# Optimization experiments

Measured on AMD Instinct MI355X. Metric: run time of the kernel, lower is better.

The kernel has to match this reference:

```python
import jax, jax.numpy as jnp
import numpy as np

N = 50000      # nodes
E = 800000     # edges (avg degree 16)
IN = 128       # in_channels
OUT = 128      # out_channels


def setup_inputs() -> dict:
    key = jax.random.key(0)
    k1, k2, k3 = jax.random.split(key, 3)
    x = jax.random.normal(k1, (N, IN), dtype=jnp.float32)
    edge_index = jax.random.randint(k2, (2, E), 0, N, dtype=jnp.int32)
    # GCNConv params: glorot-ish linear weight + zero bias
    W = jax.random.normal(k3, (IN, OUT), dtype=jnp.float32) / np.float32(np.sqrt(IN))
    b = jnp.zeros((OUT,), dtype=jnp.float32)
    return {"x": x, "W": W, "b": b, "edge_index": edge_index}


def reference(x, W, b, edge_index):
    n = x.shape[0]
    src, dst = edge_index[0], edge_index[1]
    # add self loops (GCNConv default add_self_loops=True)
    loop = jnp.arange(n, dtype=edge_index.dtype)
    src = jnp.concatenate([src, loop])
    dst = jnp.concatenate([dst, loop])
    # symmetric normalization: deg^{-1/2}[src] * deg^{-1/2}[dst], deg from dst (flow source_to_target)
    deg = jax.ops.segment_sum(jnp.ones_like(dst, dtype=x.dtype), dst, num_segments=n)
    dinv = jnp.where(deg > 0, jax.lax.rsqrt(jnp.maximum(deg, 1.0)), 0.0)
    norm = dinv[src] * dinv[dst]                     # [E+N]
    xw = x @ W                                       # [N, OUT] dense GEMM first (as GCNConv does)
    msg = xw[src] * norm[:, None]                    # [E+N, OUT] gather + scale
    out = jax.ops.segment_sum(msg, dst, num_segments=n)  # scatter-add aggregate
    return out + b
```

## Files before the change

### kernel.cpp

```cpp
#include <hip/hip_runtime.h>


constexpr int CH = 128;
constexpr int CHUNK = 4096;
constexpr int NCMAX = 256;
constexpr int HP = 256;

typedef __attribute__((ext_vector_type(8))) short short8;
typedef __attribute__((ext_vector_type(4))) float f32x4;

static __device__ __forceinline__ ushort f2bf(float f) {
    unsigned u = __float_as_uint(f);
    u += 0x7fff + ((u >> 16) & 1);
    return (ushort)(u >> 16);
}


__global__ __launch_bounds__(256) void hist_kernel(const int* __restrict__ dst,
        int* __restrict__ h, int* __restrict__ coltot, int E, int nc, int nblk) {
    __shared__ int hh[NCMAX];
    int t = threadIdx.x, b = blockIdx.x;
    for (int i = t; i < NCMAX; i += 256) hh[i] = 0;
    __syncthreads();
    int s = b * CHUNK, e = min(E, s + CHUNK);
    for (int i = s + t * 4; i < e; i += 1024) {
        if (i + 4 <= e) {
            int4 v = *(const int4*)&dst[i];
            atomicAdd(&hh[v.x >> 8], 1);
            atomicAdd(&hh[v.y >> 8], 1);
            atomicAdd(&hh[v.z >> 8], 1);
            atomicAdd(&hh[v.w >> 8], 1);
        } else {
            for (int k = i; k < e; ++k) atomicAdd(&hh[dst[k] >> 8], 1);
        }
    }
    __syncthreads();
    for (int i = t; i < nc; i += 256) {
        int v = hh[i];
        h[(size_t)i * HP + b] = v;
        if (v) atomicAdd(&coltot[i], v);
    }
}

__global__ __launch_bounds__(256) void binscatter_kernel(const int* __restrict__ src,
        const int* __restrict__ dst, const int* __restrict__ h,
        const int* __restrict__ coltot, unsigned* __restrict__ ebuf,
        int E, int nc, int nblk) {
    __shared__ int smc[256];
    __shared__ int cur[NCMAX];
    int t = threadIdx.x, b = blockIdx.x;

    smc[t] = (t < nc) ? coltot[t] : 0;
    __syncthreads();
    #pragma unroll
    for (int d = 1; d < 256; d <<= 1) {
        int u = (t >= d) ? smc[t - d] : 0;
        __syncthreads();
        smc[t] += u;
        __syncthreads();
    }
    if (t < nc) {
        int base = (t > 0) ? smc[t - 1] : 0;
        const int* hp = &h[(size_t)t * HP];
        int pfx = 0;
        int j = 0;
        for (; j + 4 <= b; j += 4) {
            int4 v = *(const int4*)&hp[j];
            pfx += v.x + v.y + v.z + v.w;
        }
        for (; j < b; ++j) pfx += hp[j];
        cur[t] = base + pfx;
    }
    __syncthreads();
    int s = b * CHUNK, e = min(E, s + CHUNK);
    for (int i = s + t; i < e; i += 256) {
        int d = dst[i];
        int pos = atomicAdd(&cur[d >> 8], 1);
        ebuf[pos] = (unsigned)src[i] | ((unsigned)(d & 255) << 16);
    }
}

__global__ __launch_bounds__(256) void bucket_csr_packw(const unsigned* __restrict__ ebuf,
        const int* __restrict__ coltot, int* __restrict__ off, ushort* __restrict__ csr,
        float* __restrict__ dinv, const float* __restrict__ Wm, ushort* __restrict__ Wp,
        int N, int nc) {
    __shared__ int hist2[256], cur[256], sm[256];
    int t = threadIdx.x, k = blockIdx.x;
    if (k >= nc) {
        int tid = (k - nc) * 256 + t;
        if (tid < 2048) {
            int col = tid >> 4, ch16 = tid & 15;
            ushort tmp[8];
            #pragma unroll
            for (int i = 0; i < 8; ++i)
                tmp[i] = f2bf(Wm[(size_t)(ch16 * 8 + i) * CH + col]);
            int d = col * 16 + (ch16 ^ (col & 7));
            *(uint4*)&Wp[(size_t)d * 8] = *(uint4*)tmp;
        }
        return;
    }
    sm[t] = (t < nc) ? coltot[t] : 0;
    __syncthreads();
    #pragma unroll
    for (int d = 1; d < 256; d <<= 1) {
        int u = (t >= d) ? sm[t - d] : 0;
        __syncthreads();
        sm[t] += u;
        __syncthreads();
    }
    int s = (k > 0) ? sm[k - 1] : 0;
    int e = sm[k];
    __syncthreads();

    hist2[t] = 0;
    __syncthreads();
    for (int i = s + t; i < e; i += 256) atomicAdd(&hist2[(ebuf[i] >> 16) & 255], 1);
    __syncthreads();
    int v = hist2[t];
    sm[t] = v;
    __syncthreads();
    #pragma unroll
    for (int d = 1; d < 256; d <<= 1) {
        int u = (t >= d) ? sm[t - d] : 0;
        __syncthreads();
        sm[t] += u;
        __syncthreads();
    }
    int excl = sm[t] - v;
    int node = k * 256 + t;
    if (node <= N) off[node] = s + excl;
    if (node < N) dinv[node] = rsqrtf((float)(v + 1));
    cur[t] = s + excl;
    __syncthreads();
    for (int i = s + t; i < e; i += 256) {
        unsigned u = ebuf[i];
        int pos = atomicAdd(&cur[(u >> 16) & 255], 1);
        csr[pos] = (ushort)(u & 0xffffu);
    }
}


__global__ __launch_bounds__(256) void gemm_mfma(const float* __restrict__ x,
        const ushort* __restrict__ Wp, const float* __restrict__ dinv,
        ushort* __restrict__ xwd, int N) {
    __shared__ alignas(16) ushort Wlds[16384];
    int t = threadIdx.x;
    int wv = t >> 6, l = t & 63;
    int c15 = l & 15, kc = l >> 4;
    int row0 = blockIdx.x * 64 + wv * 16;
    int r = row0 + c15;
    bool valid = r < N;

    short8 af[4];
    #pragma unroll
    for (int ks = 0; ks < 4; ++ks) {
        float4 a0 = make_float4(0.f,0.f,0.f,0.f), a1 = a0;
        if (valid) {
            const float* p = x + (size_t)r * CH + ks * 32 + kc * 8;
            a0 = *(const float4*)p;
            a1 = *(const float4*)(p + 4);
        }
        short8 v;
        v[0]=f2bf(a0.x); v[1]=f2bf(a0.y); v[2]=f2bf(a0.z); v[3]=f2bf(a0.w);
        v[4]=f2bf(a1.x); v[5]=f2bf(a1.y); v[6]=f2bf(a1.z); v[7]=f2bf(a1.w);
        af[ks] = v;
    }

    #pragma unroll
    for (int i = 0; i < 8; ++i) {
        int idx = i * 256 + t;
        *(uint4*)&Wlds[idx * 8] = *(const uint4*)&Wp[idx * 8];
    }
    __syncthreads();

    f32x4 acc[8];
    #pragma unroll
    for (int ct = 0; ct < 8; ++ct) { f32x4 z = {0.f,0.f,0.f,0.f}; acc[ct] = z; }

    int swz = l & 7;
    #pragma unroll
    for (int ks = 0; ks < 4; ++ks) {
        #pragma unroll
        for (int ct = 0; ct < 8; ++ct) {
            int col = ct * 16 + c15;
            int idx16 = (col * 16 + ks * 4 + kc) ^ swz;
            short8 bfrag = *(const short8*)&Wlds[idx16 * 8];
            acc[ct] = __builtin_amdgcn_mfma_f32_16x16x32_bf16(af[ks], bfrag, acc[ct], 0, 0, 0);
        }
    }

    float dv[4];
    #pragma unroll
    for (int rr = 0; rr < 4; ++rr) {
        int row = row0 + kc * 4 + rr;
        dv[rr] = (row < N) ? dinv[row] : 0.f;
    }
    __syncthreads();

    ushort* bw = Wlds + wv * 2048;
    #pragma unroll
    for (int ct = 0; ct < 8; ++ct) {
        #pragma unroll
        for (int rr = 0; rr < 4; ++rr) {
            int row_local = kc * 4 + rr;
            bw[row_local * CH + ct * 16 + c15] = f2bf(acc[ct][rr] * dv[rr]);
        }
    }
    #pragma unroll
    for (int p = 0; p < 4; ++p) {
        int row_local = p * 4 + kc;
        int row = row0 + row_local;
        if (row < N) {
            uint4 vv = *(const uint4*)&bw[row_local * CH + c15 * 8];
            *(uint4*)&xwd[(size_t)row * CH + c15 * 8] = vv;
        }
    }
}


__global__ __launch_bounds__(256) void agg_kernel(const ushort* __restrict__ xwd,
        const ushort* __restrict__ csr, const int* __restrict__ off,
        const float* __restrict__ dinv, const float* __restrict__ b,
        float* __restrict__ out, int N) {
    int t = threadIdx.x;
    int c15 = t & 15;
    int node = blockIdx.x * 16 + (t >> 4);
    if (node >= N) return;
    int s = off[node], e = off[node + 1];
    float acc[8] = {0.f,0.f,0.f,0.f,0.f,0.f,0.f,0.f};
    const ushort* base = xwd + c15 * 8;

    int last = e - 1;
    for (int j = s; j < e; j += 8) {
        int idx[8]; float m[8];
        #pragma unroll
        for (int k = 0; k < 8; ++k) {
            int jj = j + k;
            idx[k] = csr[min(jj, last)];
            m[k] = (jj <= last) ? 1.0f : 0.0f;
        }
        uint4 v[8];
        #pragma unroll
        for (int k = 0; k < 8; ++k)
            v[k] = *(const uint4*)(base + (size_t)idx[k] * CH);
        #pragma unroll
        for (int k = 0; k < 8; ++k) {
            acc[0] += m[k] * __uint_as_float(v[k].x << 16);
            acc[1] += m[k] * __uint_as_float(v[k].x & 0xffff0000u);
            acc[2] += m[k] * __uint_as_float(v[k].y << 16);
            acc[3] += m[k] * __uint_as_float(v[k].y & 0xffff0000u);
            acc[4] += m[k] * __uint_as_float(v[k].z << 16);
            acc[5] += m[k] * __uint_as_float(v[k].z & 0xffff0000u);
            acc[6] += m[k] * __uint_as_float(v[k].w << 16);
            acc[7] += m[k] * __uint_as_float(v[k].w & 0xffff0000u);
        }
    }
    {
        uint4 v = *(const uint4*)(base + (size_t)node * CH);
        acc[0] += __uint_as_float(v.x << 16);
        acc[1] += __uint_as_float(v.x & 0xffff0000u);
        acc[2] += __uint_as_float(v.y << 16);
        acc[3] += __uint_as_float(v.y & 0xffff0000u);
        acc[4] += __uint_as_float(v.z << 16);
        acc[5] += __uint_as_float(v.z & 0xffff0000u);
        acc[6] += __uint_as_float(v.w << 16);
        acc[7] += __uint_as_float(v.w & 0xffff0000u);
    }
    float di = dinv[node];
    float4 b0 = *(const float4*)&b[c15 * 8];
    float4 b1 = *(const float4*)&b[c15 * 8 + 4];
    f32x4 o0, o1;
    o0[0] = di * acc[0] + b0.x;  o0[1] = di * acc[1] + b0.y;
    o0[2] = di * acc[2] + b0.z;  o0[3] = di * acc[3] + b0.w;
    o1[0] = di * acc[4] + b1.x;  o1[1] = di * acc[5] + b1.y;
    o1[2] = di * acc[6] + b1.z;  o1[3] = di * acc[7] + b1.w;
    float* op = out + (size_t)node * CH + c15 * 8;
    __builtin_nontemporal_store(o0, (f32x4*)op);
    __builtin_nontemporal_store(o1, (f32x4*)(op + 4));
}


extern "C" void kernel_launch(void* const* d_in, const int* in_sizes, int n_in,
                              void* d_out, int out_size, void* d_ws, size_t ws_size,
                              hipStream_t stream) {
    const float* x  = (const float*)d_in[0];
    const float* Wm = (const float*)d_in[1];
    const float* b  = (const float*)d_in[2];
    const int*   ei = (const int*)d_in[3];
    int N = in_sizes[0] / CH;
    int E = in_sizes[3] / 2;
    const int* src = ei;
    const int* dst = ei + E;
    float* out = (float*)d_out;

    char* w = (char*)d_ws;
    auto alloc = [&](size_t bytes) {
        char* p = w;
        w += (bytes + 255) & ~(size_t)255;
        return p;
    };
    int nc = (N + 255) >> 8;
    int nblk = (E + CHUNK - 1) / CHUNK;

    ushort*   xwd  = (ushort*)alloc((size_t)N * CH * 2);
    unsigned* ebuf = (unsigned*)xwd;
    int*      off  = (int*)alloc((size_t)(N + 1) * 4);
    ushort*   csr  = (ushort*)alloc((size_t)E * 2);
    float*    dinv = (float*)alloc((size_t)N * 4);
    ushort*   Wp   = (ushort*)alloc((size_t)16384 * 2);
    int*      h    = (int*)alloc((size_t)nc * HP * 4);
    int*      coltot=(int*)alloc((size_t)nc * 4);

    (void)hipMemsetAsync(coltot, 0, (size_t)nc * 4, stream);
    hist_kernel<<<nblk, 256, 0, stream>>>(dst, h, coltot, E, nc, nblk);
    binscatter_kernel<<<nblk, 256, 0, stream>>>(src, dst, h, coltot, ebuf, E, nc, nblk);
    bucket_csr_packw<<<nc + 8, 256, 0, stream>>>(ebuf, coltot, off, csr, dinv, Wm, Wp, N, nc);
    gemm_mfma<<<(N + 63) / 64, 256, 0, stream>>>(x, Wp, dinv, xwd, N);
    agg_kernel<<<(N + 15) / 16, 256, 0, stream>>>(xwd, csr, off, dinv, b, out, N);
}
```

Before: 84.80 us.

## Fuse GEMM with edge binning and apply source normalization in aggregation

The dinv[src] scaling moves out of the GEMM epilogue and into the aggregation loop, applied per neighbor through an extra dinv gather. With that dependency gone, the GEMM no longer waits for the CSR build, so it runs in the same launch as the binscatter blocks and W packing joins the histogram launch. This removes one kernel launch and lets GEMM overlap with the edge scatter. The costs are a separate ebuf allocation instead of aliasing xwd, one extra scattered dinv load per edge in aggregation, and bf16 xwd now stored unscaled.

After: 86.06 us. About the same (+1.5%).

```diff
diff --git a/kernel.cpp b/kernel.cpp
--- a/kernel.cpp
+++ b/kernel.cpp
@@ -16,10 +16,25 @@
 }
 
 
-__global__ __launch_bounds__(256) void hist_kernel(const int* __restrict__ dst,
-        int* __restrict__ h, int* __restrict__ coltot, int E, int nc, int nblk) {
+__global__ __launch_bounds__(256) void hist_packw(const int* __restrict__ dst,
+        int* __restrict__ h, int* __restrict__ coltot,
+        const float* __restrict__ Wm, ushort* __restrict__ Wp,
+        int E, int nc, int nblk) {
+    int t = threadIdx.x, b = blockIdx.x;
+    if (b >= nblk) {
+        int tid = (b - nblk) * 256 + t;
+        if (tid < 2048) {
+            int col = tid >> 4, ch16 = tid & 15;
+            ushort tmp[8];
+            #pragma unroll
+            for (int i = 0; i < 8; ++i)
+                tmp[i] = f2bf(Wm[(size_t)(ch16 * 8 + i) * CH + col]);
+            int d = col * 16 + (ch16 ^ (col & 7));
+            *(uint4*)&Wp[(size_t)d * 8] = *(uint4*)tmp;
+        }
+        return;
+    }
     __shared__ int hh[NCMAX];
-    int t = threadIdx.x, b = blockIdx.x;
     for (int i = t; i < NCMAX; i += 256) hh[i] = 0;
     __syncthreads();
     int s = b * CHUNK, e = min(E, s + CHUNK);
@@ -42,112 +57,53 @@
     }
 }
 
-__global__ __launch_bounds__(256) void binscatter_kernel(const int* __restrict__ src,
+
+__global__ __launch_bounds__(256) void binscatter_gemm(const int* __restrict__ src,
         const int* __restrict__ dst, const int* __restrict__ h,
         const int* __restrict__ coltot, unsigned* __restrict__ ebuf,
-        int E, int nc, int nblk) {
-    __shared__ int smc[256];
-    __shared__ int cur[NCMAX];
+        const float* __restrict__ x, const ushort* __restrict__ Wp,
+        ushort* __restrict__ xwd, int E, int N, int nc, int nblk) {
+    __shared__ alignas(16) ushort Wlds[16384];
     int t = threadIdx.x, b = blockIdx.x;
 
-    smc[t] = (t < nc) ? coltot[t] : 0;
-    __syncthreads();
-    #pragma unroll
-    for (int d = 1; d < 256; d <<= 1) {
-        int u = (t >= d) ? smc[t - d] : 0;
-        __syncthreads();
-        smc[t] += u;
-        __syncthreads();
-    }
-    if (t < nc) {
-        int base = (t > 0) ? smc[t - 1] : 0;
-        const int* hp = &h[(size_t)t * HP];
-        int pfx = 0;
-        int j = 0;
-        for (; j + 4 <= b; j += 4) {
-            int4 v = *(const int4*)&hp[j];
-            pfx += v.x + v.y + v.z + v.w;
-        }
-        for (; j < b; ++j) pfx += hp[j];
-        cur[t] = base + pfx;
-    }
-    __syncthreads();
-    int s = b * CHUNK, e = min(E, s + CHUNK);
-    for (int i = s + t; i < e; i += 256) {
-        int d = dst[i];
-        int pos = atomicAdd(&cur[d >> 8], 1);
-        ebuf[pos] = (unsigned)src[i] | ((unsigned)(d & 255) << 16);
-    }
-}
-
-__global__ __launch_bounds__(256) void bucket_csr_packw(const unsigned* __restrict__ ebuf,
-        const int* __restrict__ coltot, int* __restrict__ off, ushort* __restrict__ csr,
-        float* __restrict__ dinv, const float* __restrict__ Wm, ushort* __restrict__ Wp,
-        int N, int nc) {
-    __shared__ int hist2[256], cur[256], sm[256];
-    int t = threadIdx.x, k = blockIdx.x;
-    if (k >= nc) {
-        int tid = (k - nc) * 256 + t;
-        if (tid < 2048) {
-            int col = tid >> 4, ch16 = tid & 15;
-            ushort tmp[8];
-            #pragma unroll
-            for (int i = 0; i < 8; ++i)
-                tmp[i] = f2bf(Wm[(size_t)(ch16 * 8 + i) * CH + col]);
-            int d = col * 16 + (ch16 ^ (col & 7));
-            *(uint4*)&Wp[(size_t)d * 8] = *(uint4*)tmp;
+    if (b < nblk) {
+        int* smc = (int*)Wlds;
+        int* cur = smc + 256;
+        smc[t] = (t < nc) ? coltot[t] : 0;
+        __syncthreads();
+        #pragma unroll
+        for (int d = 1; d < 256; d <<= 1) {
+            int u = (t >= d) ? smc[t - d] : 0;
+            __syncthreads();
+            smc[t] += u;
+            __syncthreads();
+        }
+        if (t < nc) {
+            int base = (t > 0) ? smc[t - 1] : 0;
+            const int* hp = &h[(size_t)t * HP];
+            int pfx = 0;
+            int j = 0;
+            for (; j + 4 <= b; j += 4) {
+                int4 v = *(const int4*)&hp[j];
+                pfx += v.x + v.y + v.z + v.w;
+            }
+            for (; j < b; ++j) pfx += hp[j];
+            cur[t] = base + pfx;
+        }
+        __syncthreads();
+        int s = b * CHUNK, e = min(E, s + CHUNK);
+        for (int i = s + t; i < e; i += 256) {
+            int d = dst[i];
+            int pos = atomicAdd(&cur[d >> 8], 1);
+            ebuf[pos] = (unsigned)src[i] | ((unsigned)(d & 255) << 16);
         }
         return;
     }
-    sm[t] = (t < nc) ? coltot[t] : 0;
-    __syncthreads();
-    #pragma unroll
-    for (int d = 1; d < 256; d <<= 1) {
-        int u = (t >= d) ? sm[t - d] : 0;
-        __syncthreads();
-        sm[t] += u;
-        __syncthreads();
-    }
-    int s = (k > 0) ? sm[k - 1] : 0;
-    int e = sm[k];
-    __syncthreads();
-
-    hist2[t] = 0;
-    __syncthreads();
-    for (int i = s + t; i < e; i += 256) atomicAdd(&hist2[(ebuf[i] >> 16) & 255], 1);
-    __syncthreads();
-    int v = hist2[t];
-    sm[t] = v;
-    __syncthreads();
-    #pragma unroll
-    for (int d = 1; d < 256; d <<= 1) {
-        int u = (t >= d) ? sm[t - d] : 0;
-        __syncthreads();
-        sm[t] += u;
-        __syncthreads();
-    }
-    int excl = sm[t] - v;
-    int node = k * 256 + t;
-    if (node <= N) off[node] = s + excl;
-    if (node < N) dinv[node] = rsqrtf((float)(v + 1));
-    cur[t] = s + excl;
-    __syncthreads();
-    for (int i = s + t; i < e; i += 256) {
-        unsigned u = ebuf[i];
-        int pos = atomicAdd(&cur[(u >> 16) & 255], 1);
-        csr[pos] = (ushort)(u & 0xffffu);
-    }
-}
-
-
-__global__ __launch_bounds__(256) void gemm_mfma(const float* __restrict__ x,
-        const ushort* __restrict__ Wp, const float* __restrict__ dinv,
-        ushort* __restrict__ xwd, int N) {
-    __shared__ alignas(16) ushort Wlds[16384];
-    int t = threadIdx.x;
+
+    int gb = b - nblk;
     int wv = t >> 6, l = t & 63;
     int c15 = l & 15, kc = l >> 4;
-    int row0 = blockIdx.x * 64 + wv * 16;
+    int row0 = gb * 64 + wv * 16;
     int r = row0 + c15;
     bool valid = r < N;
 
@@ -188,13 +144,6 @@
             acc[ct] = __builtin_amdgcn_mfma_f32_16x16x32_bf16(af[ks], bfrag, acc[ct], 0, 0, 0);
         }
     }
-
-    float dv[4];
-    #pragma unroll
-    for (int rr = 0; rr < 4; ++rr) {
-        int row = row0 + kc * 4 + rr;
-        dv[rr] = (row < N) ? dinv[row] : 0.f;
-    }
     __syncthreads();
 
     ushort* bw = Wlds + wv * 2048;
@@ -203,7 +152,7 @@
         #pragma unroll
         for (int rr = 0; rr < 4; ++rr) {
             int row_local = kc * 4 + rr;
-            bw[row_local * CH + ct * 16 + c15] = f2bf(acc[ct][rr] * dv[rr]);
+            bw[row_local * CH + ct * 16 + c15] = f2bf(acc[ct][rr]);
         }
     }
     #pragma unroll
@@ -214,6 +163,52 @@
             uint4 vv = *(const uint4*)&bw[row_local * CH + c15 * 8];
             *(uint4*)&xwd[(size_t)row * CH + c15 * 8] = vv;
         }
+    }
+}
+
+
+__global__ __launch_bounds__(256) void bucket_csr(const unsigned* __restrict__ ebuf,
+        const int* __restrict__ coltot, int* __restrict__ off, ushort* __restrict__ csr,
+        float* __restrict__ dinv, int N, int nc) {
+    __shared__ int hist2[256], cur[256], sm[256];
+    int t = threadIdx.x, k = blockIdx.x;
+    sm[t] = (t < nc) ? coltot[t] : 0;
+    __syncthreads();
+    #pragma unroll
+    for (int d = 1; d < 256; d <<= 1) {
+        int u = (t >= d) ? sm[t - d] : 0;
+        __syncthreads();
+        sm[t] += u;
+        __syncthreads();
+    }
+    int s = (k > 0) ? sm[k - 1] : 0;
+    int e = sm[k];
+    __syncthreads();
+
+    hist2[t] = 0;
+    __syncthreads();
+    for (int i = s + t; i < e; i += 256) atomicAdd(&hist2[(ebuf[i] >> 16) & 255], 1);
+    __syncthreads();
+    int v = hist2[t];
+    sm[t] = v;
+    __syncthreads();
+    #pragma unroll
+    for (int d = 1; d < 256; d <<= 1) {
+        int u = (t >= d) ? sm[t - d] : 0;
+        __syncthreads();
+        sm[t] += u;
+        __syncthreads();
+    }
+    int excl = sm[t] - v;
+    int node = k * 256 + t;
+    if (node <= N) off[node] = s + excl;
+    if (node < N) dinv[node] = rsqrtf((float)(v + 1));
+    cur[t] = s + excl;
+    __syncthreads();
+    for (int i = s + t; i < e; i += 256) {
+        unsigned u = ebuf[i];
+        int pos = atomicAdd(&cur[(u >> 16) & 255], 1);
+        csr[pos] = (ushort)(u & 0xffffu);
     }
 }
 
@@ -229,6 +224,7 @@
     int s = off[node], e = off[node + 1];
     float acc[8] = {0.f,0.f,0.f,0.f,0.f,0.f,0.f,0.f};
     const ushort* base = xwd + c15 * 8;
+    float di = dinv[node];
 
     int last = e - 1;
     for (int j = s; j < e; j += 8) {
@@ -237,7 +233,7 @@
         for (int k = 0; k < 8; ++k) {
             int jj = j + k;
             idx[k] = csr[min(jj, last)];
-            m[k] = (jj <= last) ? 1.0f : 0.0f;
+            m[k] = (jj <= last) ? dinv[idx[k]] : 0.0f;
         }
         uint4 v[8];
         #pragma unroll
@@ -257,16 +253,15 @@
     }
     {
         uint4 v = *(const uint4*)(base + (size_t)node * CH);
-        acc[0] += __uint_as_float(v.x << 16);
-        acc[1] += __uint_as_float(v.x & 0xffff0000u);
-        acc[2] += __uint_as_float(v.y << 16);
-        acc[3] += __uint_as_float(v.y & 0xffff0000u);
-        acc[4] += __uint_as_float(v.z << 16);
-        acc[5] += __uint_as_float(v.z & 0xffff0000u);
-        acc[6] += __uint_as_float(v.w << 16);
-        acc[7] += __uint_as_float(v.w & 0xffff0000u);
-    }
-    float di = dinv[node];
+        acc[0] += di * __uint_as_float(v.x << 16);
+        acc[1] += di * __uint_as_float(v.x & 0xffff0000u);
+        acc[2] += di * __uint_as_float(v.y << 16);
+        acc[3] += di * __uint_as_float(v.y & 0xffff0000u);
+        acc[4] += di * __uint_as_float(v.z << 16);
+        acc[5] += di * __uint_as_float(v.z & 0xffff0000u);
+        acc[6] += di * __uint_as_float(v.w << 16);
+        acc[7] += di * __uint_as_float(v.w & 0xffff0000u);
+    }
     float4 b0 = *(const float4*)&b[c15 * 8];
     float4 b1 = *(const float4*)&b[c15 * 8 + 4];
     f32x4 o0, o1;
@@ -301,9 +296,10 @@
     };
     int nc = (N + 255) >> 8;
     int nblk = (E + CHUNK - 1) / CHUNK;
+    int gemm_blocks = (N + 63) / 64;
 
     ushort*   xwd  = (ushort*)alloc((size_t)N * CH * 2);
-    unsigned* ebuf = (unsigned*)xwd;
+    unsigned* ebuf = (unsigned*)alloc((size_t)E * 4);
     int*      off  = (int*)alloc((size_t)(N + 1) * 4);
     ushort*   csr  = (ushort*)alloc((size_t)E * 2);
     float*    dinv = (float*)alloc((size_t)N * 4);
@@ -312,9 +308,9 @@
     int*      coltot=(int*)alloc((size_t)nc * 4);
 
     (void)hipMemsetAsync(coltot, 0, (size_t)nc * 4, stream);
-    hist_kernel<<<nblk, 256, 0, stream>>>(dst, h, coltot, E, nc, nblk);
-    binscatter_kernel<<<nblk, 256, 0, stream>>>(src, dst, h, coltot, ebuf, E, nc, nblk);
-    bucket_csr_packw<<<nc + 8, 256, 0, stream>>>(ebuf, coltot, off, csr, dinv, Wm, Wp, N, nc);
-    gemm_mfma<<<(N + 63) / 64, 256, 0, stream>>>(x, Wp, dinv, xwd, N);
+    hist_packw<<<nblk + 8, 256, 0, stream>>>(dst, h, coltot, Wm, Wp, E, nc, nblk);
+    binscatter_gemm<<<nblk + gemm_blocks, 256, 0, stream>>>(src, dst, h, coltot, ebuf,
+                                                            x, Wp, xwd, E, N, nc, nblk);
+    bucket_csr<<<nc, 256, 0, stream>>>(ebuf, coltot, off, csr, dinv, N, nc);
     agg_kernel<<<(N + 15) / 16, 256, 0, stream>>>(xwd, csr, off, dinv, b, out, N);
 }
```
